# Kernel optimization log

Measured on AMD Instinct MI355X. Metric: run time of the kernel, lower is better.

## Reference

```python
import jax, jax.numpy as jnp
import numpy as np

OS = 14            # output_size
GRID = 2           # ceil(roi_size/OS) = ceil(28/14) = 2 (boxes are built 28x28, sampling_ratio=-1)
NODES = OS * OS    # 196 graph nodes
EPS = 1e-5         # BatchNorm eps
K, B, C, H, W = 256, 4, 256, 112, 112


def _bn_relu(x, g, b, m, v):
    # eval-mode BatchNorm2d followed by ReLU (bn_act_conv prefix)
    s = jax.lax.rsqrt(v + EPS)
    xn = (x - m[None, :, None, None]) * s[None, :, None, None]
    return jax.nn.relu(xn * g[None, :, None, None] + b[None, :, None, None])


def _conv(x, w, b, pad):
    y = jax.lax.conv_general_dilated(x, w, (1, 1), [(pad, pad), (pad, pad)],
                                     dimension_numbers=('NCHW', 'OIHW', 'NCHW'))
    return y + b[None, :, None, None]


def _roi_align(sem, boxes):
    # torchvision roi_align, spatial_scale=1.0, aligned=False, sampling_ratio=-1 (static grid=2)
    Bs, Cc, Hh, Ww = sem.shape
    bidx = boxes[:, 0].astype(jnp.int32)
    x1, y1, x2, y2 = boxes[:, 1], boxes[:, 2], boxes[:, 3], boxes[:, 4]
    bw = jnp.maximum(x2 - x1, 1.0) / OS
    bh = jnp.maximum(y2 - y1, 1.0) / OS
    t = (jnp.arange(OS * GRID, dtype=sem.dtype) + 0.5) / GRID   # pw*GRID+ix collapsed
    xs = x1[:, None] + bw[:, None] * t                          # [K, 28]
    ys = y1[:, None] + bh[:, None] * t

    def prep(c, L):
        m = (c >= -1.0) & (c <= L)
        cc = jnp.clip(c, 0.0, L - 1)
        lo = jnp.floor(cc).astype(jnp.int32)
        hi = jnp.minimum(lo + 1, L - 1)
        return m, lo, hi, cc - lo

    my, yl, yh, ly = prep(ys, Hh)
    mx, xl, xh, lx = prep(xs, Ww)
    semt = jnp.transpose(sem, (0, 2, 3, 1))  # [B,H,W,C]

    def gat(ya, xa):
        return semt[bidx[:, None, None], ya[:, :, None], xa[:, None, :]]  # [K,28,28,C]

    ly_ = ly[:, :, None, None]
    lx_ = lx[:, None, :, None]
    val = (gat(yl, xl) * (1 - ly_) * (1 - lx_) + gat(yl, xh) * (1 - ly_) * lx_
           + gat(yh, xl) * ly_ * (1 - lx_) + gat(yh, xh) * ly_ * lx_)
    val = jnp.where((my[:, :, None] & mx[:, None, :])[..., None], val, 0.0)
    val = val.reshape(-1, OS, GRID, OS, GRID, Cc).mean(axis=(2, 4))  # avg over sampling grid
    return jnp.transpose(val, (0, 3, 1, 2))  # [K,C,14,14]


def _gcn_agg(A, x):
    # PyG gcn_norm on a fully-connected weighted graph (self loops already present):
    # deg[j] = sum_i A[i,j] (scatter on col); out[j] = sum_i d^-1/2[i] A[i,j] d^-1/2[j] x[i]
    deg = A.sum(axis=1)                 # [K,196]
    dis = jax.lax.rsqrt(deg)            # sigmoid weights > 0 => no zero degree
    Nrm = dis[:, :, None] * A * dis[:, None, :]
    return jnp.einsum('kij,kif->kjf', Nrm, x)


def _forward(roi_feature, semantic, boxes,
             bn_sem_g, bn_sem_b, bn_sem_m, bn_sem_v, conv_sem_w, conv_sem_b,
             bn_fpn_g, bn_fpn_b, bn_fpn_m, bn_fpn_v, conv_fpn_w, conv_fpn_b,
             bn_aff_g, bn_aff_b, bn_aff_m, bn_aff_v, conv_aff_w, conv_aff_b,
             gcn1_w, gcn1_b, gcn2_w, gcn2_b):
    roi_sem = _roi_align(semantic, boxes)                                   # [K,256,14,14]
    a = (_conv(_bn_relu(roi_sem, bn_sem_g, bn_sem_b, bn_sem_m, bn_sem_v), conv_sem_w, conv_sem_b, 1)
         + _conv(_bn_relu(roi_feature, bn_fpn_g, bn_fpn_b, bn_fpn_m, bn_fpn_v), conv_fpn_w, conv_fpn_b, 1))
    aff = _conv(_bn_relu(a, bn_aff_g, bn_aff_b, bn_aff_m, bn_aff_v), conv_aff_w, conv_aff_b, 0)
    A = jax.nn.sigmoid(aff.reshape(-1, NODES, NODES))                       # [K,196,196]
    X = roi_feature.reshape(-1, C, NODES).transpose(0, 2, 1)                # [K,196,256] node feats
    x1 = jax.nn.relu(_gcn_agg(A, X @ gcn1_w) + gcn1_b)                      # GCNConv(256,16)+ReLU
    x2 = _gcn_agg(A, x1 @ gcn2_w) + gcn2_b                                  # GCNConv(16,256)
    emb = x2.transpose(0, 2, 1).reshape(-1, C, OS, OS)
    return roi_sem + emb


def setup_inputs() -> dict:
    key = jax.random.key(0)
    ks = jax.random.split(key, 24)
    roi_feature = jax.random.normal(ks[0], (K, C, OS, OS), jnp.float32)
    semantic = jax.random.normal(ks[1], (B, C, H, W), jnp.float32)
    bidx = jax.random.randint(ks[2], (K,), 0, B).astype(jnp.float32)
    xy = jax.random.uniform(ks[3], (K, 2), jnp.float32, 0.0, float(H - 28))
    boxes = jnp.concatenate([bidx[:, None], xy, xy + 28.0], axis=1)  # (idx,x1,y1,x2,y2), 28x28 boxes

    def bn(kg, c):
        k1, k2, k3, k4 = jax.random.split(kg, 4)
        return (jax.random.normal(k1, (c,)) * 0.1 + 1.0,
                jax.random.normal(k2, (c,)) * 0.1,
                jax.random.normal(k3, (c,)) * 0.1,
                jax.random.uniform(k4, (c,), jnp.float32, 0.5, 1.5))
    bn_sem = bn(ks[4], C); bn_fpn = bn(ks[5], C); bn_aff = bn(ks[6], 64)
    inp = {
        'roi_feature': roi_feature, 'semantic': semantic, 'boxes': boxes,
        'bn_sem_g': bn_sem[0], 'bn_sem_b': bn_sem[1], 'bn_sem_m': bn_sem[2], 'bn_sem_v': bn_sem[3],
        'conv_sem_w': jax.random.normal(ks[7], (64, C, 3, 3)) * 0.02,
        'conv_sem_b': jax.random.normal(ks[8], (64,)) * 0.02,
        'bn_fpn_g': bn_fpn[0], 'bn_fpn_b': bn_fpn[1], 'bn_fpn_m': bn_fpn[2], 'bn_fpn_v': bn_fpn[3],
        'conv_fpn_w': jax.random.normal(ks[9], (64, C, 3, 3)) * 0.02,
        'conv_fpn_b': jax.random.normal(ks[10], (64,)) * 0.02,
        'bn_aff_g': bn_aff[0], 'bn_aff_b': bn_aff[1], 'bn_aff_m': bn_aff[2], 'bn_aff_v': bn_aff[3],
        'conv_aff_w': jax.random.normal(ks[11], (NODES, 64, 1, 1)) * 0.05,
        'conv_aff_b': jax.random.normal(ks[12], (NODES,)) * 0.05,
        'gcn1_w': jax.random.normal(ks[13], (C, 16)) * 0.05,
        'gcn1_b': jax.random.normal(ks[14], (16,)) * 0.05,
        'gcn2_w': jax.random.normal(ks[15], (16, C)) * 0.05,
        'gcn2_b': jax.random.normal(ks[16], (C,)) * 0.05,
    }
    return inp


def reference(roi_feature, semantic, boxes,
              bn_sem_g, bn_sem_b, bn_sem_m, bn_sem_v, conv_sem_w, conv_sem_b,
              bn_fpn_g, bn_fpn_b, bn_fpn_m, bn_fpn_v, conv_fpn_w, conv_fpn_b,
              bn_aff_g, bn_aff_b, bn_aff_m, bn_aff_v, conv_aff_w, conv_aff_b,
              gcn1_w, gcn1_b, gcn2_w, gcn2_b):
    return _forward(roi_feature, semantic, boxes,
                    bn_sem_g, bn_sem_b, bn_sem_m, bn_sem_v, conv_sem_w, conv_sem_b,
                    bn_fpn_g, bn_fpn_b, bn_fpn_m, bn_fpn_v, conv_fpn_w, conv_fpn_b,
                    bn_aff_g, bn_aff_b, bn_aff_m, bn_aff_v, conv_aff_w, conv_aff_b,
                    gcn1_w, gcn1_b, gcn2_w, gcn2_b)
```

## Files before the change

kernel.cpp:

```cpp
#include <hip/hip_runtime.h>
#include <hip/hip_bf16.h>

#define KBOX 256
#define CCH  256
#define NODES 196
#define OS 14
#define FTQ 3211264

typedef __attribute__((ext_vector_type(8))) short  bf16x8;
typedef __attribute__((ext_vector_type(8))) unsigned short u16x8;
typedef __attribute__((ext_vector_type(4))) float  f32x4;
typedef __attribute__((ext_vector_type(4))) short  s16x4;
typedef __attribute__((ext_vector_type(4))) int    i32x4;

__device__ __forceinline__ short f2bf(float x) {
  __hip_bfloat16 h = __float2bfloat16(x);
  return *reinterpret_cast<short*>(&h);
}
__device__ __forceinline__ float bf2f(unsigned short u) {
  unsigned int x = ((unsigned int)u) << 16;
  union { unsigned int i; float f; } c; c.i = x;
  return c.f;
}

#define MFMA16 __builtin_amdgcn_mfma_f32_16x16x32_bf16

__global__ __launch_bounds__(256) void prep_kernel(
    const float* __restrict__ bn_sem_g, const float* __restrict__ bn_sem_b,
    const float* __restrict__ bn_sem_m, const float* __restrict__ bn_sem_v,
    const float* __restrict__ conv_sem_w, const float* __restrict__ conv_sem_b,
    const float* __restrict__ bn_fpn_g, const float* __restrict__ bn_fpn_b,
    const float* __restrict__ bn_fpn_m, const float* __restrict__ bn_fpn_v,
    const float* __restrict__ conv_fpn_w, const float* __restrict__ conv_fpn_b,
    const float* __restrict__ bn_aff_g, const float* __restrict__ bn_aff_b,
    const float* __restrict__ bn_aff_m, const float* __restrict__ bn_aff_v,
    const float* __restrict__ conv_aff_w, const float* __restrict__ g1w,
    const float* __restrict__ g2w,
    float* __restrict__ ss_sem, float* __restrict__ ss_fpn, float* __restrict__ ss_aff2,
    short* __restrict__ wfrag, short* __restrict__ wafrag, short* __restrict__ g1wf,
    short* __restrict__ g2wf)
{
  int gid = blockIdx.x * blockDim.x + threadIdx.x;
  int gsz = gridDim.x * blockDim.x;
  for (int c = gid; c < 256; c += gsz) {
    float s = bn_sem_g[c] * rsqrtf(bn_sem_v[c] + 1e-5f);
    ss_sem[c] = s; ss_sem[256 + c] = bn_sem_b[c] - bn_sem_m[c] * s;
    float s2 = bn_fpn_g[c] * rsqrtf(bn_fpn_v[c] + 1e-5f);
    ss_fpn[c] = s2; ss_fpn[256 + c] = bn_fpn_b[c] - bn_fpn_m[c] * s2;
  }
  for (int c = gid; c < 64; c += gsz) {
    float s = bn_aff_g[c] * rsqrtf(bn_aff_v[c] + 1e-5f);
    float sh = bn_aff_b[c] - bn_aff_m[c] * s;
    float bias = conv_sem_b[c] + conv_fpn_b[c];
    ss_aff2[c] = s; ss_aff2[64 + c] = bias * s + sh;
  }
  for (int idx = gid; idx < 144 * 4 * 64 * 8; idx += gsz) {
    int e = idx & 7, lane = (idx >> 3) & 63, nt = (idx >> 9) & 3, kstep = idx >> 11;
    int src = kstep / 72, rem = kstep % 72, icc = rem / 9, pos = rem % 9;
    int ky = pos / 3, kx = pos % 3;
    int oc = nt * 16 + (lane & 15);
    int ic = icc * 32 + (lane >> 4) * 8 + e;
    const float* w = src ? conv_fpn_w : conv_sem_w;
    wfrag[idx] = f2bf(w[((oc * 256 + ic) * 3 + ky) * 3 + kx]);
  }
  for (int idx = gid; idx < 2 * 13 * 64 * 8; idx += gsz) {
    int t = idx;
    int e = t & 7; t >>= 3;
    int lane = t & 63; t >>= 6;
    int nt = t % 13; int s = t / 13;
    int i = nt * 16 + (lane & 15);
    int ic = s * 32 + (lane >> 4) * 8 + e;
    wafrag[idx] = f2bf(i < NODES ? conv_aff_w[i * 64 + ic] : 0.f);
  }
  for (int idx = gid; idx < 8 * 64 * 8; idx += gsz) {
    int e = idx & 7, lane = (idx >> 3) & 63, ks = idx >> 9;
    int ic = ks * 32 + (lane >> 4) * 8 + e;
    int f = lane & 15;
    g1wf[idx] = f2bf(g1w[ic * 16 + f]);
  }
  for (int idx = gid; idx < 16 * 64 * 8; idx += gsz) {
    int e = idx & 7, lane = (idx >> 3) & 63, ct = idx >> 9;
    int kk = (lane >> 4) * 8 + e;
    int c = ct * 16 + (lane & 15);
    g2wf[idx] = f2bf(kk < 16 ? g2w[kk * 256 + c] : 0.f);
  }
}

__global__ __launch_bounds__(256) void transpose_bf16_kernel(
    const float* __restrict__ in, unsigned short* __restrict__ out, int C, int HW)
{
  __shared__ float tile[64][65];
  int nh = (HW + 63) >> 6;
  int bi = blockIdx.x;
  int cb = bi % (C >> 6); bi /= (C >> 6);
  int hb = bi % nh; int b = bi / nh;
  int tx = threadIdx.x & 63, ty = threadIdx.x >> 6;
  const float* inb = in + (size_t)b * C * HW;
  unsigned short* outb = out + (size_t)b * HW * C;
  #pragma unroll
  for (int i = ty; i < 64; i += 4) {
    int c = cb * 64 + i, hw = hb * 64 + tx;
    tile[i][tx] = (hw < HW) ? inb[(size_t)c * HW + hw] : 0.f;
  }
  __syncthreads();
  int cp = threadIdx.x & 31;
  #pragma unroll
  for (int i = (int)(threadIdx.x >> 5); i < 64; i += 8) {
    int hw = hb * 64 + i;
    if (hw < HW) {
      ushort2 v;
      v.x = (unsigned short)f2bf(tile[cp * 2][i]);
      v.y = (unsigned short)f2bf(tile[cp * 2 + 1][i]);
      *(ushort2*)&outb[(size_t)hw * C + cb * 64 + cp * 2] = v;
    }
  }
}

__global__ __launch_bounds__(512) void roi_align_kernel(
    const unsigned short* __restrict__ semt, const float* __restrict__ boxes,
    unsigned short* __restrict__ roi_sem)
{
  __shared__ unsigned short slab[5][29][256];
  int kb = blockIdx.x / 7, g = blockIdx.x % 7;
  int tid = threadIdx.x, wave = tid >> 6, lane = tid & 63;
  const float* bx = boxes + kb * 5;
  int bb = (int)bx[0];
  float x1 = bx[1], y1 = bx[2];
  float xb = x1 + 0.5f, yv = y1 + 0.5f;
  int X0 = (int)floorf(xb); float fx = xb - (float)X0;
  int Y0 = (int)floorf(yv); float fy = yv - (float)Y0;
  const unsigned short* base = semt + (size_t)bb * 12544 * 256;
  #pragma unroll
  for (int i = 0; i < 19; ++i) {
    int s = wave + i * 8;
    if (s < 145) {
      int r = s / 29, xi = s - r * 29;
      int yr = min(Y0 + 4 * g + r, 111);
      int xc = min(X0 + xi, 111);
      *(s16x4*)&slab[r][xi][lane * 4] =
          *(const s16x4*)(base + ((size_t)yr * 112 + xc) * 256 + lane * 4);
    }
  }
  __syncthreads();
  int c2 = tid & 127, grp = tid >> 7;
  int oyl = grp >> 1, og = grp & 1;
  int rb = oyl * 2;
  float w0 = 1.f - fy;
  unsigned short* op = roi_sem + (((size_t)kb * NODES) + (2 * g + oyl) * OS) * 256 + c2 * 2;
  #pragma unroll
  for (int oxs = 0; oxs < 7; ++oxs) {
    int ox = og * 7 + oxs;
    float o0 = 0.f, o1 = 0.f;
    #pragma unroll
    for (int xi = 0; xi < 3; ++xi) {
      float xw = (xi == 0) ? (1.f - fx) : (xi == 1 ? 1.f : fx);
      const unsigned short* p0 = &slab[rb][2 * ox + xi][c2 * 2];
      const unsigned short* p1 = &slab[rb + 1][2 * ox + xi][c2 * 2];
      const unsigned short* p2 = &slab[rb + 2][2 * ox + xi][c2 * 2];
      o0 += xw * (w0 * bf2f(p0[0]) + bf2f(p1[0]) + fy * bf2f(p2[0]));
      o1 += xw * (w0 * bf2f(p0[1]) + bf2f(p1[1]) + fy * bf2f(p2[1]));
    }
    ushort2 v;
    v.x = (unsigned short)f2bf(o0 * 0.25f);
    v.y = (unsigned short)f2bf(o1 * 0.25f);
    *(ushort2*)(op + (size_t)ox * 256) = v;
  }
}

__global__ __launch_bounds__(256) void conv_ab_kernel(
    const unsigned short* __restrict__ roi_sem, const unsigned short* __restrict__ roif,
    const float* __restrict__ ss_sem, const float* __restrict__ ss_fpn,
    const short* __restrict__ wfrag, short* __restrict__ a_part)
{
  int bi = blockIdx.x;
  int k = bi >> 2, src = (bi >> 1) & 1, ih = bi & 1;
  int tid = threadIdx.x;
  int wave = tid >> 6, lane = tid & 63;
  int l15 = lane & 15, lq = lane >> 4;
  __shared__ short lds_in[197 * 36 + 4];
  __shared__ short lds_wf[18432];
  __shared__ float lds_sc[256], lds_sh[256];

  {
    const float* ss = src ? ss_fpn : ss_sem;
    lds_sc[tid] = ss[tid]; lds_sh[tid] = ss[256 + tid];
  }
  if (tid < 36) lds_in[196 * 36 + tid] = 0;

  int oyA[4], oxA[4], jA[4]; bool mvA[4];
  #pragma unroll
  for (int mi = 0; mi < 4; ++mi) {
    int mt = (mi < 3) ? (wave + mi * 4) : 12;
    mvA[mi] = (mi < 3) | (wave == 3);
    int j = mt * 16 + l15;
    jA[mi] = j;
    int oy = j / 14;
    oyA[mi] = oy; oxA[mi] = j - oy * 14;
  }

  u16x8 inv[4];
  i32x4 wv[9];
  const unsigned short* inp = (src ? roif : roi_sem) + (size_t)k * NODES * CCH;

  f32x4 acc[4][4];
  #pragma unroll
  for (int i = 0; i < 4; ++i)
    #pragma unroll
    for (int j = 0; j < 4; ++j) acc[i][j] = f32x4{0.f, 0.f, 0.f, 0.f};

#define ISSUE_LOADS(P) do {                                                  \
    int icc_ = ih * 4 + (P);                                                 \
    const unsigned short* in_ = inp + icc_ * 32;                             \
    _Pragma("unroll")                                                        \
    for (int i_ = 0; i_ < 3; ++i_) {                                         \
      int f_ = tid + i_ * 256;                                               \
      inv[i_] = *(const u16x8*)(in_ + (size_t)(f_ >> 2) * 256 + (f_ & 3) * 8); \
    }                                                                        \
    if (tid < 16) {                                                          \
      int f_ = 768 + tid;                                                    \
      inv[3] = *(const u16x8*)(in_ + (size_t)(f_ >> 2) * 256 + (f_ & 3) * 8); \
    }                                                                        \
    const i32x4* wsl_ = (const i32x4*)(wfrag + (size_t)(src * 72 + icc_ * 9) * 2048); \
    _Pragma("unroll")                                                        \
    for (int i_ = 0; i_ < 9; ++i_) wv[i_] = wsl_[tid + i_ * 256];            \
  } while (0)

#define WRITE_STAGE(P) do {                                                  \
    int icc_ = ih * 4 + (P);                                                 \
    _Pragma("unroll")                                                        \
    for (int i_ = 0; i_ < 3; ++i_) {                                         \
      int f_ = tid + i_ * 256;                                               \
      int j_ = f_ >> 2, cq_ = f_ & 3;                                        \
      bf16x8 pk_;                                                            \
      _Pragma("unroll")                                                      \
      for (int u_ = 0; u_ < 8; ++u_) {                                       \
        int c_ = icc_ * 32 + cq_ * 8 + u_;                                   \
        float x_ = bf2f(inv[i_][u_]) * lds_sc[c_] + lds_sh[c_];              \
        pk_[u_] = f2bf(fmaxf(x_, 0.f));                                      \
      }                                                                      \
      *(bf16x8*)&lds_in[j_ * 36 + cq_ * 8] = pk_;                            \
    }                                                                        \
    if (tid < 16) {                                                          \
      int f_ = 768 + tid; int j_ = f_ >> 2, cq_ = f_ & 3;                    \
      bf16x8 pk_;                                                            \
      _Pragma("unroll")                                                      \
      for (int u_ = 0; u_ < 8; ++u_) {                                       \
        int c_ = icc_ * 32 + cq_ * 8 + u_;                                   \
        float x_ = bf2f(inv[3][u_]) * lds_sc[c_] + lds_sh[c_];               \
        pk_[u_] = f2bf(fmaxf(x_, 0.f));                                      \
      }                                                                      \
      *(bf16x8*)&lds_in[j_ * 36 + cq_ * 8] = pk_;                            \
    }                                                                        \
    _Pragma("unroll")                                                        \
    for (int i_ = 0; i_ < 9; ++i_) ((i32x4*)lds_wf)[tid + i_ * 256] = wv[i_];\
  } while (0)

  ISSUE_LOADS(0);
  __syncthreads();
  WRITE_STAGE(0);

  for (int p = 0; p < 4; ++p) {
    __syncthreads();
    if (p < 3) ISSUE_LOADS(p + 1);
    #pragma unroll
    for (int pos = 0; pos < 9; ++pos) {
      int ky = pos / 3 - 1, kx = pos % 3 - 1;
      bf16x8 bfr[4];
      #pragma unroll
      for (int n = 0; n < 4; ++n)
        bfr[n] = *(const bf16x8*)&lds_wf[((pos * 4 + n) * 64 + lane) * 8];
      #pragma unroll
      for (int mi = 0; mi < 4; ++mi) {
        if (!mvA[mi]) continue;
        int ny = oyA[mi] + ky, nx = oxA[mi] + kx;
        bool v = (jA[mi] < 196) & ((unsigned)ny < 14u) & ((unsigned)nx < 14u);
        int np = v ? (ny * 14 + nx) : 196;
        bf16x8 afr = *(const bf16x8*)&lds_in[np * 36 + lq * 8];
        acc[mi][0] = MFMA16(afr, bfr[0], acc[mi][0], 0, 0, 0);
        acc[mi][1] = MFMA16(afr, bfr[1], acc[mi][1], 0, 0, 0);
        acc[mi][2] = MFMA16(afr, bfr[2], acc[mi][2], 0, 0, 0);
        acc[mi][3] = MFMA16(afr, bfr[3], acc[mi][3], 0, 0, 0);
      }
    }
    __syncthreads();
    if (p < 3) WRITE_STAGE(p + 1);
  }

  short* op = a_part + (size_t)(src * 2 + ih) * FTQ;
  #pragma unroll
  for (int mi = 0; mi < 4; ++mi) {
    if (!mvA[mi]) continue;
    int mt = (mi < 3) ? (wave + mi * 4) : 12;
    #pragma unroll
    for (int n = 0; n < 4; ++n) {
      int oc = n * 16 + l15;
      #pragma unroll
      for (int r = 0; r < 4; ++r) {
        int j = mt * 16 + lq * 4 + r;
        if (j < NODES)
          op[((size_t)k * NODES + j) * 64 + oc] = f2bf(acc[mi][n][r]);
      }
    }
  }
#undef ISSUE_LOADS
#undef WRITE_STAGE
}

__global__ __launch_bounds__(1024, 1) void graph_kernel(
    const short* __restrict__ a_part, const float* __restrict__ ss_aff2,
    const short* __restrict__ wafrag,
    const float* __restrict__ aff_b, const short* __restrict__ g1wf,
    const float* __restrict__ g1b, const unsigned short* __restrict__ roif_bf,
    const short* __restrict__ g2wf, const float* __restrict__ g2b,
    const unsigned short* __restrict__ roi_sem, float* __restrict__ outp)
{
  __shared__ __align__(16) char smem[125840];
  const int tid = threadIdx.x, wave = tid >> 6, lane = tid & 63;
  const int l15 = lane & 15, lq = lane >> 4;
  const int k = blockIdx.x;

  char*  Ab   = smem;
  short* wa   = (short*)(smem + 96512);
  short* yfr  = (short*)(smem + 96512);
  short* zsf  = (short*)(smem + 103680);
  float* dsl  = (float*)(smem + 123136);
  float* g1bl = (float*)(smem + 123968);
  float* g2bl = (float*)(smem + 124032);
  float* affb = (float*)(smem + 125056);

  const bool wv13 = (wave < 13);
  const int jr  = wave * 16 + l15;
  const int jrc = min(jr, 195);
  const i32x4 z4 = {};

  bf16x8 af0 = {}, af1 = {};
  if (wv13) {
    float s0[8] = {0,0,0,0,0,0,0,0}, s1[8] = {0,0,0,0,0,0,0,0};
    #pragma unroll
    for (int sl = 0; sl < 4; ++sl) {
      const unsigned short* p = (const unsigned short*)a_part + (size_t)sl * FTQ
                                + ((size_t)k * NODES + jrc) * 64 + lq * 8;
      u16x8 v0 = *(const u16x8*)p;
      u16x8 v1 = *(const u16x8*)(p + 32);
      #pragma unroll
      for (int e = 0; e < 8; ++e) { s0[e] += bf2f(v0[e]); s1[e] += bf2f(v1[e]); }
    }
    #pragma unroll
    for (int e = 0; e < 8; ++e) {
      int oc0 = lq * 8 + e, oc1 = 32 + lq * 8 + e;
      af0[e] = f2bf(fmaxf(s0[e] * ss_aff2[oc0] + ss_aff2[64 + oc0], 0.f));
      af1[e] = f2bf(fmaxf(s1[e] * ss_aff2[oc1] + ss_aff2[64 + oc1], 0.f));
    }
  }
  {
    i32x4 w0 = ((const i32x4*)wafrag)[tid];
    i32x4 w1 = z4;
    if (tid < 640) w1 = ((const i32x4*)wafrag)[1024 + tid];
    if (tid < 832) {
      int r = tid >> 2, q = tid & 3;
      *(i32x4*)(Ab + r * 464 + 384 + q * 16) = z4;
    }
    if (tid < 196) affb[tid] = aff_b[tid];
    if (tid < 256) g2bl[tid] = g2b[tid];
    if (tid < 16)  g1bl[tid] = g1b[tid];
    ((i32x4*)wa)[tid] = w0;
    if (tid < 640) ((i32x4*)wa)[1024 + tid] = w1;
  }
  __syncthreads();

  if (wv13) {
    float rsum[4] = {0.f, 0.f, 0.f, 0.f};
    #pragma unroll
    for (int n = 0; n < 13; ++n) {
      bf16x8 b0 = *(const bf16x8*)(wa + (n * 64 + lane) * 8);
      bf16x8 b1 = *(const bf16x8*)(wa + ((13 + n) * 64 + lane) * 8);
      f32x4 acc = {0.f, 0.f, 0.f, 0.f};
      acc = MFMA16(af0, b0, acc, 0, 0, 0);
      acc = MFMA16(af1, b1, acc, 0, 0, 0);
      int i = n * 16 + l15;
      bool iv = (i < 196);
      float bv = affb[iv ? i : 0];
      #pragma unroll
      for (int r = 0; r < 4; ++r) {
        float v = acc[r] + bv;
        float s = 1.f / (1.f + __expf(-v));
        if (iv) {
          rsum[r] += s;
          *(short*)(Ab + (wave * 16 + lq * 4 + r) * 464 + i * 2) = f2bf(s);
        }
      }
    }
    #pragma unroll
    for (int r = 0; r < 4; ++r) {
      float v = rsum[r];
      v += __shfl_xor(v, 1); v += __shfl_xor(v, 2);
      v += __shfl_xor(v, 4); v += __shfl_xor(v, 8);
      int j = wave * 16 + lq * 4 + r;
      if (l15 == 0 && j < 196) dsl[j] = rsqrtf(v);
    }
  }
  __syncthreads();

  *(i32x4*)(smem + 96512 + tid * 16) = z4;
  if (tid < 256) *(i32x4*)(smem + 96512 + (1024 + tid) * 16) = z4;
  f32x4 xacc = {0.f, 0.f, 0.f, 0.f};
  if (wv13) {
    const unsigned short* Xp = roif_bf + (size_t)k * 50176 + (size_t)jrc * 256 + lq * 8;
    #pragma unroll
    for (int ks = 0; ks < 8; ++ks) {
      bf16x8 xa = *(const bf16x8*)(Xp + ks * 32);
      bf16x8 xb = *(const bf16x8*)(g1wf + (ks * 64 + lane) * 8);
      xacc = MFMA16(xa, xb, xacc, 0, 0, 0);
    }
  }
  __syncthreads();

  if (wv13) {
    #pragma unroll
    for (int r = 0; r < 4; ++r) {
      int i = wave * 16 + lq * 4 + r;
      if (i < 196) {
        float yv = dsl[i] * xacc[r];
        yfr[((i >> 5) * 64 + ((i >> 3) & 3) * 16 + l15) * 8 + (i & 7)] = f2bf(yv);
      }
    }
  }
  __syncthreads();

  f32x4 g0 = {0.f, 0.f, 0.f, 0.f};
  if (wv13) {
    #pragma unroll
    for (int ks = 0; ks < 7; ++ks) {
      bf16x8 bb = *(const bf16x8*)(yfr + (ks * 64 + lane) * 8);
      bf16x8 a0 = *(const bf16x8*)(Ab + jr * 464 + ks * 64 + lq * 16);
      g0 = MFMA16(a0, bb, g0, 0, 0, 0);
    }
  }
  __syncthreads();
  if (wv13) {
    #pragma unroll
    for (int r = 0; r < 4; ++r) {
      int i = wave * 16 + lq * 4 + r;
      if (i < 196) {
        float d = dsl[i];
        float x1v = fmaxf(g0[r] * d + g1bl[l15], 0.f);
        yfr[((i >> 5) * 64 + ((i >> 3) & 3) * 16 + l15) * 8 + (i & 7)] = f2bf(d * x1v);
      }
    }
  }
  __syncthreads();

  if (wv13) {
    f32x4 z0 = {0.f, 0.f, 0.f, 0.f};
    #pragma unroll
    for (int ks = 0; ks < 7; ++ks) {
      bf16x8 bb = *(const bf16x8*)(yfr + (ks * 64 + lane) * 8);
      bf16x8 a0 = *(const bf16x8*)(Ab + jr * 464 + ks * 64 + lq * 16);
      z0 = MFMA16(a0, bb, z0, 0, 0, 0);
    }
    #pragma unroll
    for (int r = 0; r < 4; ++r) {
      int j = wave * 16 + lq * 4 + r;
      if (j < 196) {
        float zv = z0[r] * dsl[j];
        zsf[((j >> 4) * 64 + (l15 >> 3) * 16 + (j & 15)) * 8 + (l15 & 7)] = f2bf(zv);
      }
    }
  }
  __syncthreads();

  {
    bf16x8 wf = *(const bf16x8*)(g2wf + (wave * 64 + lane) * 8);
    const unsigned short* rsmk = roi_sem + (size_t)k * 50176;
    float* op = outp + (size_t)k * 50176;
    unsigned short* rst = (unsigned short*)smem;
    const int c_ = wave * 16 + lq * 4;
    float gbv[4];
    #pragma unroll
    for (int r = 0; r < 4; ++r) gbv[r] = g2bl[c_ + r];
    #pragma unroll
    for (int it = 0; it < 3; ++it) {
      int v = tid + it * 1024;
      int row = v >> 5, cq = v & 31;
      *(u16x8*)&rst[row * 264 + cq * 8] = *(const u16x8*)(rsmk + (size_t)row * 256 + cq * 8);
    }
    __syncthreads();
    #pragma unroll
    for (int jt = 0; jt < 6; ++jt) {
      bf16x8 zb = *(const bf16x8*)(zsf + (jt * 64 + lane) * 8);
      f32x4 d = {0.f, 0.f, 0.f, 0.f};
      d = MFMA16(wf, zb, d, 0, 0, 0);
      int j = jt * 16 + l15;
      const unsigned short* rr = rst + j * 264 + c_;
      unsigned int p01 = *(const unsigned int*)rr;
      unsigned int p23 = *(const unsigned int*)(rr + 2);
      op[(size_t)(c_ + 0) * 196 + j] = d[0] + gbv[0] + bf2f((unsigned short)(p01 & 0xffff));
      op[(size_t)(c_ + 1) * 196 + j] = d[1] + gbv[1] + bf2f((unsigned short)(p01 >> 16));
      op[(size_t)(c_ + 2) * 196 + j] = d[2] + gbv[2] + bf2f((unsigned short)(p23 & 0xffff));
      op[(size_t)(c_ + 3) * 196 + j] = d[3] + gbv[3] + bf2f((unsigned short)(p23 >> 16));
    }
    __syncthreads();
    #pragma unroll
    for (int it = 0; it < 4; ++it) {
      int v = tid + it * 1024;
      if (v < 3200) {
        int row = v >> 5, cq = v & 31;
        *(u16x8*)&rst[row * 264 + cq * 8] = *(const u16x8*)(rsmk + (size_t)(96 + row) * 256 + cq * 8);
      }
    }
    __syncthreads();
    #pragma unroll
    for (int jt = 6; jt < 13; ++jt) {
      bf16x8 zb = *(const bf16x8*)(zsf + (jt * 64 + lane) * 8);
      f32x4 d = {0.f, 0.f, 0.f, 0.f};
      d = MFMA16(wf, zb, d, 0, 0, 0);
      int j = jt * 16 + l15;
      if (j < 196) {
        const unsigned short* rr = rst + (j - 96) * 264 + c_;
        unsigned int p01 = *(const unsigned int*)rr;
        unsigned int p23 = *(const unsigned int*)(rr + 2);
        op[(size_t)(c_ + 0) * 196 + j] = d[0] + gbv[0] + bf2f((unsigned short)(p01 & 0xffff));
        op[(size_t)(c_ + 1) * 196 + j] = d[1] + gbv[1] + bf2f((unsigned short)(p01 >> 16));
        op[(size_t)(c_ + 2) * 196 + j] = d[2] + gbv[2] + bf2f((unsigned short)(p23 & 0xffff));
        op[(size_t)(c_ + 3) * 196 + j] = d[3] + gbv[3] + bf2f((unsigned short)(p23 >> 16));
      }
    }
  }
}

extern "C" void kernel_launch(void* const* d_in, const int* in_sizes, int n_in,
                              void* d_out, int out_size, void* d_ws, size_t ws_size,
                              hipStream_t stream) {
  const float* roi_feature = (const float*)d_in[0];
  const float* semantic    = (const float*)d_in[1];
  const float* boxes       = (const float*)d_in[2];
  const float* bn_sem_g = (const float*)d_in[3];
  const float* bn_sem_b = (const float*)d_in[4];
  const float* bn_sem_m = (const float*)d_in[5];
  const float* bn_sem_v = (const float*)d_in[6];
  const float* conv_sem_w = (const float*)d_in[7];
  const float* conv_sem_b = (const float*)d_in[8];
  const float* bn_fpn_g = (const float*)d_in[9];
  const float* bn_fpn_b = (const float*)d_in[10];
  const float* bn_fpn_m = (const float*)d_in[11];
  const float* bn_fpn_v = (const float*)d_in[12];
  const float* conv_fpn_w = (const float*)d_in[13];
  const float* conv_fpn_b = (const float*)d_in[14];
  const float* bn_aff_g = (const float*)d_in[15];
  const float* bn_aff_b = (const float*)d_in[16];
  const float* bn_aff_m = (const float*)d_in[17];
  const float* bn_aff_v = (const float*)d_in[18];
  const float* conv_aff_w = (const float*)d_in[19];
  const float* conv_aff_b = (const float*)d_in[20];
  const float* gcn1_w = (const float*)d_in[21];
  const float* gcn1_b = (const float*)d_in[22];
  const float* gcn2_w = (const float*)d_in[23];
  const float* gcn2_b = (const float*)d_in[24];

  const size_t FT = (size_t)KBOX * NODES * CCH;
  unsigned short* ws16      = (unsigned short*)d_ws;
  unsigned short* semt_bf   = ws16;
  unsigned short* roif_bf   = semt_bf + FT;
  unsigned short* roi_sem_b = roif_bf + FT;
  short*          a_part    = (short*)(roi_sem_b + FT);
  float*          ss_sem    = (float*)(a_part + 4 * (size_t)FTQ);
  float*          ss_fpn    = ss_sem + 512;
  float*          ss_aff2   = ss_fpn + 512;
  short*          wfrag     = (short*)(ss_aff2 + 128);
  short*          wafrag    = wfrag + 294912;
  short*          g1wf      = wafrag + 13312;
  short*          g2wf      = g1wf + 4096;

  prep_kernel<<<256, 256, 0, stream>>>(
      bn_sem_g, bn_sem_b, bn_sem_m, bn_sem_v, conv_sem_w, conv_sem_b,
      bn_fpn_g, bn_fpn_b, bn_fpn_m, bn_fpn_v, conv_fpn_w, conv_fpn_b,
      bn_aff_g, bn_aff_b, bn_aff_m, bn_aff_v, conv_aff_w, gcn1_w, gcn2_w,
      ss_sem, ss_fpn, ss_aff2, wfrag, wafrag, g1wf, g2wf);

  transpose_bf16_kernel<<<4 * 196 * 4, 256, 0, stream>>>(semantic, semt_bf, 256, 12544);
  transpose_bf16_kernel<<<4 * 4 * 256, 256, 0, stream>>>(roi_feature, roif_bf, 256, 196);
  roi_align_kernel<<<KBOX * 7, 512, 0, stream>>>(semt_bf, boxes, roi_sem_b);
  conv_ab_kernel<<<KBOX * 4, 256, 0, stream>>>(roi_sem_b, roif_bf, ss_sem, ss_fpn, wfrag, a_part);
  graph_kernel<<<KBOX, 1024, 0, stream>>>(a_part, ss_aff2, wafrag, conv_aff_b, g1wf, gcn1_b,
                                          roif_bf, g2wf, gcn2_b, roi_sem_b, (float*)d_out);
}
```

Measured before the change: 145.3 us.

## Drop conv input-channel split, pad LDS rows, prefetch roi_sem in graph kernel

The conv_ab kernel no longer splits the input channels into two halves across blocks. Each block now loops over all 8 channel chunks, so it writes one partial tensor instead of two, and the graph kernel sums 2 partials instead of 4. The LDS input row stride grows from 36 to 40 shorts, which changes the bank mapping of the A-fragment reads. The graph kernel also loads the roi_sem rows into registers before they are staged, overlapping global latency with the MFMA work. In exchange, half as many conv blocks run, each doing twice as much serial work, which lowers parallelism.

```diff
diff --git a/kernel.cpp b/kernel.cpp
--- a/kernel.cpp
+++ b/kernel.cpp
@@ -173,11 +173,11 @@
     const short* __restrict__ wfrag, short* __restrict__ a_part)
 {
   int bi = blockIdx.x;
-  int k = bi >> 2, src = (bi >> 1) & 1, ih = bi & 1;
+  int k = bi >> 1, src = bi & 1;
   int tid = threadIdx.x;
   int wave = tid >> 6, lane = tid & 63;
   int l15 = lane & 15, lq = lane >> 4;
-  __shared__ short lds_in[197 * 36 + 4];
+  __shared__ short lds_in[197][40];
   __shared__ short lds_wf[18432];
   __shared__ float lds_sc[256], lds_sh[256];
 
@@ -185,7 +185,7 @@
     const float* ss = src ? ss_fpn : ss_sem;
     lds_sc[tid] = ss[tid]; lds_sh[tid] = ss[256 + tid];
   }
-  if (tid < 36) lds_in[196 * 36 + tid] = 0;
+  if (tid < 40) lds_in[196][tid] = 0;
 
   int oyA[4], oxA[4], jA[4]; bool mvA[4];
   #pragma unroll
@@ -201,6 +201,7 @@
   u16x8 inv[4];
   i32x4 wv[9];
   const unsigned short* inp = (src ? roif : roi_sem) + (size_t)k * NODES * CCH;
+  const short* wbase = wfrag + (size_t)src * 72 * 2048;
 
   f32x4 acc[4][4];
   #pragma unroll
@@ -209,7 +210,7 @@
     for (int j = 0; j < 4; ++j) acc[i][j] = f32x4{0.f, 0.f, 0.f, 0.f};
 
 #define ISSUE_LOADS(P) do {                                                  \
-    int icc_ = ih * 4 + (P);                                                 \
+    int icc_ = (P);                                                          \
     const unsigned short* in_ = inp + icc_ * 32;                             \
     _Pragma("unroll")                                                        \
     for (int i_ = 0; i_ < 3; ++i_) {                                         \
@@ -220,13 +221,13 @@
       int f_ = 768 + tid;                                                    \
       inv[3] = *(const u16x8*)(in_ + (size_t)(f_ >> 2) * 256 + (f_ & 3) * 8); \
     }                                                                        \
-    const i32x4* wsl_ = (const i32x4*)(wfrag + (size_t)(src * 72 + icc_ * 9) * 2048); \
+    const i32x4* wsl_ = (const i32x4*)(wbase + (size_t)icc_ * 9 * 2048);     \
     _Pragma("unroll")                                                        \
     for (int i_ = 0; i_ < 9; ++i_) wv[i_] = wsl_[tid + i_ * 256];            \
   } while (0)
 
 #define WRITE_STAGE(P) do {                                                  \
-    int icc_ = ih * 4 + (P);                                                 \
+    int icc_ = (P);                                                          \
     _Pragma("unroll")                                                        \
     for (int i_ = 0; i_ < 3; ++i_) {                                         \
       int f_ = tid + i_ * 256;                                               \
@@ -238,7 +239,7 @@
         float x_ = bf2f(inv[i_][u_]) * lds_sc[c_] + lds_sh[c_];              \
         pk_[u_] = f2bf(fmaxf(x_, 0.f));                                      \
       }                                                                      \
-      *(bf16x8*)&lds_in[j_ * 36 + cq_ * 8] = pk_;                            \
+      *(bf16x8*)&lds_in[j_][cq_ * 8] = pk_;                                  \
     }                                                                        \
     if (tid < 16) {                                                          \
       int f_ = 768 + tid; int j_ = f_ >> 2, cq_ = f_ & 3;                    \
@@ -249,7 +250,7 @@
         float x_ = bf2f(inv[3][u_]) * lds_sc[c_] + lds_sh[c_];               \
         pk_[u_] = f2bf(fmaxf(x_, 0.f));                                      \
       }                                                                      \
-      *(bf16x8*)&lds_in[j_ * 36 + cq_ * 8] = pk_;                            \
+      *(bf16x8*)&lds_in[j_][cq_ * 8] = pk_;                                  \
     }                                                                        \
     _Pragma("unroll")                                                        \
     for (int i_ = 0; i_ < 9; ++i_) ((i32x4*)lds_wf)[tid + i_ * 256] = wv[i_];\
@@ -259,9 +260,9 @@
   __syncthreads();
   WRITE_STAGE(0);
 
-  for (int p = 0; p < 4; ++p) {
+  for (int p = 0; p < 8; ++p) {
     __syncthreads();
-    if (p < 3) ISSUE_LOADS(p + 1);
+    if (p < 7) ISSUE_LOADS(p + 1);
     #pragma unroll
     for (int pos = 0; pos < 9; ++pos) {
       int ky = pos / 3 - 1, kx = pos % 3 - 1;
@@ -275,7 +276,7 @@
         int ny = oyA[mi] + ky, nx = oxA[mi] + kx;
         bool v = (jA[mi] < 196) & ((unsigned)ny < 14u) & ((unsigned)nx < 14u);
         int np = v ? (ny * 14 + nx) : 196;
-        bf16x8 afr = *(const bf16x8*)&lds_in[np * 36 + lq * 8];
+        bf16x8 afr = *(const bf16x8*)&lds_in[np][lq * 8];
         acc[mi][0] = MFMA16(afr, bfr[0], acc[mi][0], 0, 0, 0);
         acc[mi][1] = MFMA16(afr, bfr[1], acc[mi][1], 0, 0, 0);
         acc[mi][2] = MFMA16(afr, bfr[2], acc[mi][2], 0, 0, 0);
@@ -283,10 +284,10 @@
       }
     }
     __syncthreads();
-    if (p < 3) WRITE_STAGE(p + 1);
-  }
-
-  short* op = a_part + (size_t)(src * 2 + ih) * FTQ;
+    if (p < 7) WRITE_STAGE(p + 1);
+  }
+
+  short* op = a_part + (size_t)src * FTQ;
   #pragma unroll
   for (int mi = 0; mi < 4; ++mi) {
     if (!mvA[mi]) continue;
@@ -332,12 +333,13 @@
   const int jr  = wave * 16 + l15;
   const int jrc = min(jr, 195);
   const i32x4 z4 = {};
+  const unsigned short* rsmk = roi_sem + (size_t)k * 50176;
 
   bf16x8 af0 = {}, af1 = {};
   if (wv13) {
     float s0[8] = {0,0,0,0,0,0,0,0}, s1[8] = {0,0,0,0,0,0,0,0};
     #pragma unroll
-    for (int sl = 0; sl < 4; ++sl) {
+    for (int sl = 0; sl < 2; ++sl) {
       const unsigned short* p = (const unsigned short*)a_part + (size_t)sl * FTQ
                                 + ((size_t)k * NODES + jrc) * 64 + lq * 8;
       u16x8 v0 = *(const u16x8*)p;
@@ -450,6 +452,14 @@
   }
   __syncthreads();
 
+  u16x8 pre0[3];
+  #pragma unroll
+  for (int it = 0; it < 3; ++it) {
+    int v = tid + it * 1024;
+    int row = v >> 5, cq = v & 31;
+    pre0[it] = *(const u16x8*)(rsmk + (size_t)row * 256 + cq * 8);
+  }
+
   if (wv13) {
     f32x4 z0 = {0.f, 0.f, 0.f, 0.f};
     #pragma unroll
@@ -471,7 +481,6 @@
 
   {
     bf16x8 wf = *(const bf16x8*)(g2wf + (wave * 64 + lane) * 8);
-    const unsigned short* rsmk = roi_sem + (size_t)k * 50176;
     float* op = outp + (size_t)k * 50176;
     unsigned short* rst = (unsigned short*)smem;
     const int c_ = wave * 16 + lq * 4;
@@ -482,9 +491,18 @@
     for (int it = 0; it < 3; ++it) {
       int v = tid + it * 1024;
       int row = v >> 5, cq = v & 31;
-      *(u16x8*)&rst[row * 264 + cq * 8] = *(const u16x8*)(rsmk + (size_t)row * 256 + cq * 8);
+      *(u16x8*)&rst[row * 264 + cq * 8] = pre0[it];
     }
     __syncthreads();
+    u16x8 pre1[4];
+    #pragma unroll
+    for (int it = 0; it < 4; ++it) {
+      int v = tid + it * 1024;
+      if (v < 3200) {
+        int row = v >> 5, cq = v & 31;
+        pre1[it] = *(const u16x8*)(rsmk + (size_t)(96 + row) * 256 + cq * 8);
+      }
+    }
     #pragma unroll
     for (int jt = 0; jt < 6; ++jt) {
       bf16x8 zb = *(const bf16x8*)(zsf + (jt * 64 + lane) * 8);
@@ -505,7 +523,7 @@
       int v = tid + it * 1024;
       if (v < 3200) {
         int row = v >> 5, cq = v & 31;
-        *(u16x8*)&rst[row * 264 + cq * 8] = *(const u16x8*)(rsmk + (size_t)(96 + row) * 256 + cq * 8);
+        *(u16x8*)&rst[row * 264 + cq * 8] = pre1[it];
       }
     }
     __syncthreads();
@@ -563,7 +581,7 @@
   unsigned short* roif_bf   = semt_bf + FT;
   unsigned short* roi_sem_b = roif_bf + FT;
   short*          a_part    = (short*)(roi_sem_b + FT);
-  float*          ss_sem    = (float*)(a_part + 4 * (size_t)FTQ);
+  float*          ss_sem    = (float*)(a_part + 2 * (size_t)FTQ);
   float*          ss_fpn    = ss_sem + 512;
   float*          ss_aff2   = ss_fpn + 512;
   short*          wfrag     = (short*)(ss_aff2 + 128);
@@ -580,7 +598,7 @@
   transpose_bf16_kernel<<<4 * 196 * 4, 256, 0, stream>>>(semantic, semt_bf, 256, 12544);
   transpose_bf16_kernel<<<4 * 4 * 256, 256, 0, stream>>>(roi_feature, roif_bf, 256, 196);
   roi_align_kernel<<<KBOX * 7, 512, 0, stream>>>(semt_bf, boxes, roi_sem_b);
-  conv_ab_kernel<<<KBOX * 4, 256, 0, stream>>>(roi_sem_b, roif_bf, ss_sem, ss_fpn, wfrag, a_part);
+  conv_ab_kernel<<<KBOX * 2, 256, 0, stream>>>(roi_sem_b, roif_bf, ss_sem, ss_fpn, wfrag, a_part);
   graph_kernel<<<KBOX, 1024, 0, stream>>>(a_part, ss_aff2, wafrag, conv_aff_b, g1wf, gcn1_b,
                                           roif_bf, g2wf, gcn2_b, roi_sem_b, (float*)d_out);
 }
```

New measurement: 136.0 us. 1.07x faster.
